# Optimization experiments

Hardware: AMD Instinct MI355X
Metric: run time of the kernel (lower is better)

The kernel has to match this reference:

```python
import jax, jax.numpy as jnp
import numpy as np

N = 1_000_000   # total nodes
G = 10_000      # graphs (100 nodes each)
K = 30          # sortpool k = min(30, N//G)
F_IN = 64
LAT = [64, 64, 64, 34]
OUT = 2


def setup_inputs() -> dict:
    key = jax.random.key(0)
    ks = jax.random.split(key, 20)
    s = 0.02
    inp = {
        "x": jax.random.normal(ks[0], (N, F_IN), jnp.float32),
        "edge_index": jax.random.randint(ks[1], (2, 1_000_000), 0, N, dtype=jnp.int32),
        "batch": (jnp.arange(N, dtype=jnp.int32) // (N // G)).astype(jnp.int32),
        # MLP stack params (torch Linear: [out, in])
        "W1": s * jax.random.normal(ks[2], (LAT[0], F_IN), jnp.float32),
        "b1": jnp.zeros((LAT[0],), jnp.float32),
        "W2": s * jax.random.normal(ks[3], (LAT[1], LAT[0]), jnp.float32),
        "b2": jnp.zeros((LAT[1],), jnp.float32),
        "W3": s * jax.random.normal(ks[4], (LAT[2], LAT[1]), jnp.float32),
        "b3": jnp.zeros((LAT[2],), jnp.float32),
        "W4": s * jax.random.normal(ks[5], (LAT[3], LAT[2]), jnp.float32),
        "b4": jnp.zeros((LAT[3],), jnp.float32),
        # Conv1d params (torch: [out_ch, in_ch, kernel])
        "cw1": s * jax.random.normal(ks[6], (16, 1, 5), jnp.float32),
        "cb1": jnp.zeros((16,), jnp.float32),
        "cw2": s * jax.random.normal(ks[7], (32, 16, 5), jnp.float32),
        "cb2": jnp.zeros((32,), jnp.float32),
        # dense head: dense_dim = ((30-2)//2+1 - 5 + 1)*32 = 352
        "Wo": s * jax.random.normal(ks[8], (OUT, 352), jnp.float32),
        "bo": jnp.zeros((OUT,), jnp.float32),
    }
    return inp


def _dgcnn_fwd(x, batch, W1, b1, W2, b2, W3, b3, W4, b4, cw1, cb1, cw2, cb2, Wo, bo):
    # per-node MLP stack
    h = jax.nn.relu(x @ W1.T + b1)
    h = jax.nn.relu(h @ W2.T + b2)
    h = jax.nn.relu(h @ W3.T + b3)
    h = jax.nn.relu(h @ W4.T + b4)  # [N, 34]
    # mean over the FIRST K nodes of each (contiguous, sorted) graph segment
    ones = jnp.ones((h.shape[0],), h.dtype)
    counts = jax.ops.segment_sum(ones, batch, num_segments=G)          # [G]
    starts = jnp.cumsum(counts) - counts                                # segment start offsets
    pos = jnp.arange(h.shape[0], dtype=h.dtype) - starts[batch]         # position within segment
    mask = (pos < K).astype(h.dtype)                                    # first K nodes
    sums = jax.ops.segment_sum(h * mask[:, None], batch, num_segments=G)
    denom = jnp.minimum(counts, jnp.asarray(K, h.dtype))
    pooled = sums / denom[:, None]                                       # [G, 34]
    # conv1d stages (latent_dim[-1]=34 >= 5, so no adaptive pooling branch)
    h = pooled[:, None, :]  # [G, 1, 34]
    dn = ('NCH', 'OIH', 'NCH')
    h = jax.nn.relu(jax.lax.conv_general_dilated(h, cw1, (1,), 'VALID', dimension_numbers=dn) + cb1[None, :, None])  # [G,16,30]
    h = jax.lax.reduce_window(h, -jnp.inf, jax.lax.max, (1, 1, 2), (1, 1, 2), 'VALID')                               # [G,16,15]
    h = jax.nn.relu(jax.lax.conv_general_dilated(h, cw2, (1,), 'VALID', dimension_numbers=dn) + cb2[None, :, None])  # [G,32,11]
    h = h.reshape(h.shape[0], -1)  # [G, 352]
    return h @ Wo.T + bo           # [G, OUT]


def reference(x, edge_index, batch, W1, b1, W2, b2, W3, b3, W4, b4, cw1, cb1, cw2, cb2, Wo, bo):
    # edge_index is accepted but unused by the original forward
    return _dgcnn_fwd(x, batch, W1, b1, W2, b2, W3, b3, W4, b4, cw1, cb1, cw2, cb2, Wo, bo)
```

## Files before the change

kernel.cpp:

```cpp
#include <hip/hip_runtime.h>


#define GRAPHS 10000

__global__ void transpose_cw2_k(const float* __restrict__ cw2, float* __restrict__ cwT) {
  int idx = blockIdx.x * 256 + threadIdx.x;
  if (idx < 2560) {
    int o = idx / 80;
    int r = idx % 80;
    cwT[r * 32 + o] = cw2[idx];
  }
}

__device__ __forceinline__ float dot64(const float* __restrict__ wr, const float (&xx)[64]) {
  float a0 = 0.f, a1 = 0.f, a2 = 0.f, a3 = 0.f;
  #pragma unroll
  for (int k = 0; k < 64; k += 4) {
    a0 = fmaf(wr[k+0], xx[k+0], a0);
    a1 = fmaf(wr[k+1], xx[k+1], a1);
    a2 = fmaf(wr[k+2], xx[k+2], a2);
    a3 = fmaf(wr[k+3], xx[k+3], a3);
  }
  return (a0 + a1) + (a2 + a3);
}

__device__ __forceinline__ void half_layer32(const float* __restrict__ W,
                                             const float* __restrict__ b,
                                             const float (&in)[64],
                                             float* __restrict__ acol, int j0) {
  #pragma unroll 2
  for (int jj = 0; jj < 32; ++jj) {
    const int j = j0 + jj;
    float v = dot64(W + j * 64, in) + b[j];
    acol[j * 64] = v > 0.f ? v : 0.f;
  }
}

__device__ __forceinline__ void copy_back(float (&in)[64], const float* __restrict__ acol) {
  #pragma unroll
  for (int k = 0; k < 64; ++k) in[k] = acol[k * 64];
}

__global__ __launch_bounds__(256, 1) void dgcnn_main(
    const float* __restrict__ x,
    const float* __restrict__ W1, const float* __restrict__ b1,
    const float* __restrict__ W2, const float* __restrict__ b2,
    const float* __restrict__ W3, const float* __restrict__ b3,
    const float* __restrict__ W4, const float* __restrict__ b4,
    const float* __restrict__ cw1, const float* __restrict__ cb1,
    const float* __restrict__ cw2t, const float* __restrict__ cw2,
    const float* __restrict__ cb2,
    const float* __restrict__ Wo, const float* __restrict__ bo,
    float* __restrict__ out, int use_t)
{
  __shared__ float act[2][64 * 64];
  __shared__ float pooled[2][2][34];
  __shared__ float mbuf[2][2][240];

  const int tid  = threadIdx.x;
  const int grp  = tid >> 7;
  const int wig  = (tid >> 6) & 1;
  const int lane = tid & 63;
  const int half = lane >> 5;
  const int pos  = lane & 31;
  const int gidx = blockIdx.x * 2 + grp;
  const int g    = gidx * 2 + half;
  const long node = (long)g * 100 + pos;

  const int j0 = __builtin_amdgcn_readfirstlane(wig << 5);
  const int j4 = __builtin_amdgcn_readfirstlane(wig * 17);

  float* const acol = &act[grp][lane];

  float in[64];
  const float4* xv = (const float4*)(x + node * 64);
  #pragma unroll
  for (int i = 0; i < 16; ++i) {
    float4 v = xv[i];
    in[4*i+0] = v.x; in[4*i+1] = v.y; in[4*i+2] = v.z; in[4*i+3] = v.w;
  }

  half_layer32(W1, b1, in, acol, j0);
  __syncthreads();
  copy_back(in, acol);
  __syncthreads();
  half_layer32(W2, b2, in, acol, j0);
  __syncthreads();
  copy_back(in, acol);
  __syncthreads();
  half_layer32(W3, b3, in, acol, j0);
  __syncthreads();
  copy_back(in, acol);

  const float inv30 = 1.0f / 30.0f;
  #pragma unroll 2
  for (int jj = 0; jj < 17; ++jj) {
    const int j = j4 + jj;
    float v = dot64(W4 + j * 64, in) + b4[j];
    v = v > 0.f ? v : 0.f;
    if (pos >= 30) v = 0.f;
    #pragma unroll
    for (int off = 16; off >= 1; off >>= 1) v += __shfl_xor(v, off);
    if (pos == 0) pooled[grp][half][j] = v * inv30;
  }
  __syncthreads();

  const int gw = gidx * 2 + wig;

  if (lane < 16) {
    const int c = lane;
    const float* P = pooled[grp][wig];
    float w0 = cw1[c*5+0], w1 = cw1[c*5+1], w2 = cw1[c*5+2], w3 = cw1[c*5+3], w4 = cw1[c*5+4];
    float bb = cb1[c];
    #pragma unroll
    for (int q = 0; q < 15; ++q) {
      int p = 2 * q;
      float s0 = bb + w0*P[p+0] + w1*P[p+1] + w2*P[p+2] + w3*P[p+3] + w4*P[p+4];
      float s1 = bb + w0*P[p+1] + w1*P[p+2] + w2*P[p+3] + w3*P[p+4] + w4*P[p+5];
      mbuf[grp][wig][c * 15 + q] = fmaxf(fmaxf(s0, s1), 0.f);
    }
  }

  if (lane < 32) {
    const int o = lane;
    float acc[11];
    float bb2 = cb2[o];
    #pragma unroll
    for (int p = 0; p < 11; ++p) acc[p] = bb2;
    #pragma unroll 1
    for (int i = 0; i < 16; ++i) {
      float mr[15];
      #pragma unroll
      for (int q = 0; q < 15; ++q) mr[q] = mbuf[grp][wig][i * 15 + q];
      #pragma unroll
      for (int t = 0; t < 5; ++t) {
        float wt = use_t ? cw2t[(i * 5 + t) * 32 + o]
                         : cw2[o * 80 + i * 5 + t];
        #pragma unroll
        for (int p = 0; p < 11; ++p) acc[p] = fmaf(wt, mr[p + t], acc[p]);
      }
    }

    float p0 = 0.f, p1 = 0.f;
    #pragma unroll
    for (int p = 0; p < 11; ++p) {
      float v = acc[p] > 0.f ? acc[p] : 0.f;
      p0 = fmaf(v, Wo[o * 11 + p], p0);
      p1 = fmaf(v, Wo[352 + o * 11 + p], p1);
    }
    #pragma unroll
    for (int off = 16; off >= 1; off >>= 1) {
      p0 += __shfl_xor(p0, off);
      p1 += __shfl_xor(p1, off);
    }
    if (lane == 0) {
      out[gw * 2 + 0] = p0 + bo[0];
      out[gw * 2 + 1] = p1 + bo[1];
    }
  }
}

extern "C" void kernel_launch(void* const* d_in, const int* in_sizes, int n_in,
                              void* d_out, int out_size, void* d_ws, size_t ws_size,
                              hipStream_t stream) {
  const float* x    = (const float*)d_in[0];
  const float* W1   = (const float*)d_in[3];
  const float* b1   = (const float*)d_in[4];
  const float* W2   = (const float*)d_in[5];
  const float* b2   = (const float*)d_in[6];
  const float* W3   = (const float*)d_in[7];
  const float* b3   = (const float*)d_in[8];
  const float* W4   = (const float*)d_in[9];
  const float* b4   = (const float*)d_in[10];
  const float* cw1  = (const float*)d_in[11];
  const float* cb1  = (const float*)d_in[12];
  const float* cw2  = (const float*)d_in[13];
  const float* cb2  = (const float*)d_in[14];
  const float* Wo   = (const float*)d_in[15];
  const float* bo   = (const float*)d_in[16];
  float* out = (float*)d_out;

  float* cwT = (float*)d_ws;
  int use_t = (ws_size >= 2560 * sizeof(float)) ? 1 : 0;
  if (use_t) {
    transpose_cw2_k<<<10, 256, 0, stream>>>(cw2, cwT);
  }
  dgcnn_main<<<GRAPHS / 4, 256, 0, stream>>>(
      x, W1, b1, W2, b2, W3, b3, W4, b4,
      cw1, cb1, cwT, cw2, cb2, Wo, bo, out, use_t);
}
```

Measured before the change: 692.4 us.

## Split each layer's outputs across four waves, one graph pair per block

Each block now handles 2 graphs instead of 4. The 64 output features of each MLP layer are split into four quarters of 16, one per wave, instead of two halves of 32. The last layer is split 9 features per wave with a bound guard. The 1-block-per-SM launch-bounds hint is dropped and the grid is doubled, which cuts per-thread serial dot-product work and LDS use so more blocks can be resident. The cost is that each wave still loads the full 64-float input row, so x loads and copy_back reads per useful FLOP double, and half the waves sit idle during the conv tail.

```diff
diff --git a/kernel.cpp b/kernel.cpp
--- a/kernel.cpp
+++ b/kernel.cpp
@@ -24,12 +24,12 @@
   return (a0 + a1) + (a2 + a3);
 }
 
-__device__ __forceinline__ void half_layer32(const float* __restrict__ W,
-                                             const float* __restrict__ b,
-                                             const float (&in)[64],
-                                             float* __restrict__ acol, int j0) {
+__device__ __forceinline__ void quarter_layer16(const float* __restrict__ W,
+                                                const float* __restrict__ b,
+                                                const float (&in)[64],
+                                                float* __restrict__ acol, int j0) {
   #pragma unroll 2
-  for (int jj = 0; jj < 32; ++jj) {
+  for (int jj = 0; jj < 16; ++jj) {
     const int j = j0 + jj;
     float v = dot64(W + j * 64, in) + b[j];
     acol[j * 64] = v > 0.f ? v : 0.f;
@@ -41,7 +41,7 @@
   for (int k = 0; k < 64; ++k) in[k] = acol[k * 64];
 }
 
-__global__ __launch_bounds__(256, 1) void dgcnn_main(
+__global__ __launch_bounds__(256) void dgcnn_main(
     const float* __restrict__ x,
     const float* __restrict__ W1, const float* __restrict__ b1,
     const float* __restrict__ W2, const float* __restrict__ b2,
@@ -53,24 +53,22 @@
     const float* __restrict__ Wo, const float* __restrict__ bo,
     float* __restrict__ out, int use_t)
 {
-  __shared__ float act[2][64 * 64];
-  __shared__ float pooled[2][2][34];
-  __shared__ float mbuf[2][2][240];
+  __shared__ float act[64 * 64];
+  __shared__ float pooled[2][34];
+  __shared__ float mbuf[2][240];
 
   const int tid  = threadIdx.x;
-  const int grp  = tid >> 7;
-  const int wig  = (tid >> 6) & 1;
+  const int wig  = tid >> 6;
   const int lane = tid & 63;
   const int half = lane >> 5;
   const int pos  = lane & 31;
-  const int gidx = blockIdx.x * 2 + grp;
-  const int g    = gidx * 2 + half;
+  const int g    = blockIdx.x * 2 + half;
   const long node = (long)g * 100 + pos;
 
-  const int j0 = __builtin_amdgcn_readfirstlane(wig << 5);
-  const int j4 = __builtin_amdgcn_readfirstlane(wig * 17);
+  const int j0 = __builtin_amdgcn_readfirstlane(wig << 4);
+  const int j4 = __builtin_amdgcn_readfirstlane(wig * 9);
 
-  float* const acol = &act[grp][lane];
+  float* const acol = &act[lane];
 
   float in[64];
   const float4* xv = (const float4*)(x + node * 64);
@@ -80,82 +78,86 @@
     in[4*i+0] = v.x; in[4*i+1] = v.y; in[4*i+2] = v.z; in[4*i+3] = v.w;
   }
 
-  half_layer32(W1, b1, in, acol, j0);
+  quarter_layer16(W1, b1, in, acol, j0);
   __syncthreads();
   copy_back(in, acol);
   __syncthreads();
-  half_layer32(W2, b2, in, acol, j0);
+  quarter_layer16(W2, b2, in, acol, j0);
   __syncthreads();
   copy_back(in, acol);
   __syncthreads();
-  half_layer32(W3, b3, in, acol, j0);
+  quarter_layer16(W3, b3, in, acol, j0);
   __syncthreads();
   copy_back(in, acol);
 
   const float inv30 = 1.0f / 30.0f;
   #pragma unroll 2
-  for (int jj = 0; jj < 17; ++jj) {
+  for (int jj = 0; jj < 9; ++jj) {
     const int j = j4 + jj;
-    float v = dot64(W4 + j * 64, in) + b4[j];
-    v = v > 0.f ? v : 0.f;
-    if (pos >= 30) v = 0.f;
-    #pragma unroll
-    for (int off = 16; off >= 1; off >>= 1) v += __shfl_xor(v, off);
-    if (pos == 0) pooled[grp][half][j] = v * inv30;
+    if (j < 34) {
+      float v = dot64(W4 + j * 64, in) + b4[j];
+      v = v > 0.f ? v : 0.f;
+      if (pos >= 30) v = 0.f;
+      #pragma unroll
+      for (int off = 16; off >= 1; off >>= 1) v += __shfl_xor(v, off);
+      if (pos == 0) pooled[half][j] = v * inv30;
+    }
   }
   __syncthreads();
 
-  const int gw = gidx * 2 + wig;
+  if (wig < 2) {
+    const int gw = blockIdx.x * 2 + wig;
 
-  if (lane < 16) {
-    const int c = lane;
-    const float* P = pooled[grp][wig];
-    float w0 = cw1[c*5+0], w1 = cw1[c*5+1], w2 = cw1[c*5+2], w3 = cw1[c*5+3], w4 = cw1[c*5+4];
-    float bb = cb1[c];
-    #pragma unroll
-    for (int q = 0; q < 15; ++q) {
-      int p = 2 * q;
-      float s0 = bb + w0*P[p+0] + w1*P[p+1] + w2*P[p+2] + w3*P[p+3] + w4*P[p+4];
-      float s1 = bb + w0*P[p+1] + w1*P[p+2] + w2*P[p+3] + w3*P[p+4] + w4*P[p+5];
-      mbuf[grp][wig][c * 15 + q] = fmaxf(fmaxf(s0, s1), 0.f);
-    }
-  }
-
-  if (lane < 32) {
-    const int o = lane;
-    float acc[11];
-    float bb2 = cb2[o];
-    #pragma unroll
-    for (int p = 0; p < 11; ++p) acc[p] = bb2;
-    #pragma unroll 1
-    for (int i = 0; i < 16; ++i) {
-      float mr[15];
+    if (lane < 16) {
+      const int c = lane;
+      const float* P = pooled[wig];
+      float w0 = cw1[c*5+0], w1 = cw1[c*5+1], w2 = cw1[c*5+2], w3 = cw1[c*5+3], w4 = cw1[c*5+4];
+      float bb = cb1[c];
       #pragma unroll
-      for (int q = 0; q < 15; ++q) mr[q] = mbuf[grp][wig][i * 15 + q];
-      #pragma unroll
-      for (int t = 0; t < 5; ++t) {
-        float wt = use_t ? cw2t[(i * 5 + t) * 32 + o]
-                         : cw2[o * 80 + i * 5 + t];
-        #pragma unroll
-        for (int p = 0; p < 11; ++p) acc[p] = fmaf(wt, mr[p + t], acc[p]);
+      for (int q = 0; q < 15; ++q) {
+        int p = 2 * q;
+        float s0 = bb + w0*P[p+0] + w1*P[p+1] + w2*P[p+2] + w3*P[p+3] + w4*P[p+4];
+        float s1 = bb + w0*P[p+1] + w1*P[p+2] + w2*P[p+3] + w3*P[p+4] + w4*P[p+5];
+        mbuf[wig][c * 15 + q] = fmaxf(fmaxf(s0, s1), 0.f);
       }
     }
 
-    float p0 = 0.f, p1 = 0.f;
-    #pragma unroll
-    for (int p = 0; p < 11; ++p) {
-      float v = acc[p] > 0.f ? acc[p] : 0.f;
-      p0 = fmaf(v, Wo[o * 11 + p], p0);
-      p1 = fmaf(v, Wo[352 + o * 11 + p], p1);
-    }
-    #pragma unroll
-    for (int off = 16; off >= 1; off >>= 1) {
-      p0 += __shfl_xor(p0, off);
-      p1 += __shfl_xor(p1, off);
-    }
-    if (lane == 0) {
-      out[gw * 2 + 0] = p0 + bo[0];
-      out[gw * 2 + 1] = p1 + bo[1];
+    if (lane < 32) {
+      const int o = lane;
+      float acc[11];
+      float bb2 = cb2[o];
+      #pragma unroll
+      for (int p = 0; p < 11; ++p) acc[p] = bb2;
+      #pragma unroll 1
+      for (int i = 0; i < 16; ++i) {
+        float mr[15];
+        #pragma unroll
+        for (int q = 0; q < 15; ++q) mr[q] = mbuf[wig][i * 15 + q];
+        #pragma unroll
+        for (int t = 0; t < 5; ++t) {
+          float wt = use_t ? cw2t[(i * 5 + t) * 32 + o]
+                           : cw2[o * 80 + i * 5 + t];
+          #pragma unroll
+          for (int p = 0; p < 11; ++p) acc[p] = fmaf(wt, mr[p + t], acc[p]);
+        }
+      }
+
+      float p0 = 0.f, p1 = 0.f;
+      #pragma unroll
+      for (int p = 0; p < 11; ++p) {
+        float v = acc[p] > 0.f ? acc[p] : 0.f;
+        p0 = fmaf(v, Wo[o * 11 + p], p0);
+        p1 = fmaf(v, Wo[352 + o * 11 + p], p1);
+      }
+      #pragma unroll
+      for (int off = 16; off >= 1; off >>= 1) {
+        p0 += __shfl_xor(p0, off);
+        p1 += __shfl_xor(p1, off);
+      }
+      if (lane == 0) {
+        out[gw * 2 + 0] = p0 + bo[0];
+        out[gw * 2 + 1] = p1 + bo[1];
+      }
     }
   }
 }
@@ -185,7 +187,7 @@
   if (use_t) {
     transpose_cw2_k<<<10, 256, 0, stream>>>(cw2, cwT);
   }
-  dgcnn_main<<<GRAPHS / 4, 256, 0, stream>>>(
+  dgcnn_main<<<GRAPHS / 2, 256, 0, stream>>>(
       x, W1, b1, W2, b2, W3, b3, W4, b4,
       cw1, cb1, cwT, cw2, cb2, Wo, bo, out, use_t);
 }
```

New measurement: 690.9 us. No clear change (-0.2%).
